# Kernel optimization log

Hardware: AMD Instinct MI355X
Metric: run time of the kernel (lower is better)

Reference implementation:

```python
import jax, jax.numpy as jnp
import numpy as np

B, L = 2048, 120            # batch, sentence length
V, P = 114042, 102          # word vocab, position vocab
WE, PE = 50, 5              # word / position embedding dims
F, K, R = 230, 3, 53        # filters, kernel size, relations
D = WE + 2 * PE             # feature dim = 60


def setup_inputs() -> dict:
    key = jax.random.key(0)
    ks = jax.random.split(key, 10)
    sent = jax.random.randint(ks[0], (B, L), 0, V)
    pf = jax.random.randint(ks[1], (B, 2, L), 0, P)
    # entity positions: ensure 1 <= pool0 < pool1 <= L-1 so all 3 segments are non-empty
    p0 = jax.random.randint(ks[2], (B,), 3, 40)
    p1 = jax.random.randint(ks[3], (B,), 60, 115)
    epos = jnp.stack([p0, p1], axis=1) - 1  # forward uses pool = epos + 1
    s = 0.02
    W_word = jax.random.normal(ks[4], (V, WE), jnp.float32) * s
    W_pos1 = jax.random.normal(ks[5], (P, PE), jnp.float32) * s
    W_pos2 = jax.random.normal(ks[6], (P, PE), jnp.float32) * s
    conv_w = jax.random.normal(ks[7], (F, 1, K, D), jnp.float32) * s
    conv_b = jnp.zeros((F,), jnp.float32)
    lin_w = jax.random.normal(ks[8], (R, 3 * F), jnp.float32) * s
    lin_b = jnp.zeros((R,), jnp.float32)
    return dict(sent=sent, pf=pf, epos=epos, W_word=W_word, W_pos1=W_pos1,
                W_pos2=W_pos2, conv_w=conv_w, conv_b=conv_b, lin_w=lin_w, lin_b=lin_b)


def reference(sent, pf, epos, W_word, W_pos1, W_pos2, conv_w, conv_b, lin_w, lin_b):
    # embeddings -> [B, L, D]
    emb = jnp.concatenate([W_word[sent], W_pos1[pf[:, 0]], W_pos2[pf[:, 1]]], axis=-1)
    # conv over (length, feature) with full-width kernel; dropout is identity (eval)
    x = emb[:, None, :, :]  # [B, 1, L, D]
    y = jax.lax.conv_general_dilated(x, conv_w, window_strides=(1, 1),
                                     padding=[(K // 2, K // 2), (0, 0)])  # [B, F, L, 1]
    y = jnp.tanh(y[..., 0] + conv_b[None, :, None])  # [B, F, L]
    # piecewise (3-segment) max pooling, segment boundaries per batch item
    pool = epos + 1                                   # [B, 2]
    pos = jnp.arange(L)[None, :]                      # [1, L]
    seg = (pos >= pool[:, :1]).astype(jnp.int32) + (pos >= pool[:, 1:]).astype(jnp.int32)  # [B, L] in {0,1,2}
    neg = jnp.finfo(y.dtype).min
    pooled = [jnp.max(jnp.where((seg == s)[:, None, :], y, neg), axis=2) for s in range(3)]
    feats = jnp.stack(pooled, axis=-1).reshape(B, F * 3)  # matches torch cat+view ordering
    return feats @ lin_w.T + lin_b  # [B, R]
```

## Files before the change

kernel.cpp:

```cpp
#include <hip/hip_runtime.h>
#include <math.h>

#define BB 2048
#define LL 120
#define WE_ 50
#define PE_ 5
#define DD 60
#define FF 230
#define KK 3
#define RR 53

#define NKT 6
#define NNT 15
#define NPAD 240
#define EMB_ELEMS 7936

#define WS_BP    0
#define WS_LT    92160
#define WS_EMBG  246784

#define ACC_BIAS 16.0f

#define GATHER_ITEMS (BB * LL * 30)
#define GATHER_BLKS  (GATHER_ITEMS / 256)
#define BP_ITEMS     (NNT * NKT * 64 * 8)
#define LT_ITEMS     (690 * 56)
#define PREP_BLKS    ((BP_ITEMS + LT_ITEMS + 255) / 256)

typedef __attribute__((ext_vector_type(8))) short short8_t;
typedef __attribute__((ext_vector_type(4))) short short4_t;
typedef __attribute__((ext_vector_type(4))) float float4_t;

__device__ __forceinline__ unsigned f2bf(float x) {
    unsigned u = __builtin_bit_cast(unsigned, x);
    return (u + 0x7fffu + ((u >> 16) & 1u)) >> 16;
}

__device__ __forceinline__ float tanh_fast(float x) {
    float t = __expf(2.0f * x);
    return 1.0f - 2.0f * __builtin_amdgcn_rcpf(t + 1.0f);
}

__global__ __launch_bounds__(256) void pcnn_gp(
    const int* __restrict__ sent, const int* __restrict__ pf,
    const float* __restrict__ Wword, const float* __restrict__ Wpos1,
    const float* __restrict__ Wpos2, const float* __restrict__ convw,
    const float* __restrict__ linw,
    unsigned* __restrict__ embg32, unsigned short* __restrict__ bp,
    float* __restrict__ lt)
{
    int bid = blockIdx.x;
    if (bid < GATHER_BLKS) {
        int idx = bid * 256 + threadIdx.x;
        int c  = idx % 30;
        int lc = idx / 30;
        int l  = lc % LL;
        int b  = lc / LL;
        unsigned pk;
        if (c < 25) {
            int w = sent[b * LL + l];
            float2 v = *(const float2*)(Wword + w * WE_ + 2 * c);
            pk = f2bf(v.x) | (f2bf(v.y) << 16);
        } else {
            int p = pf[b * 2 * LL + l];
            int q = pf[b * 2 * LL + LL + l];
            int j0 = (c - 25) * 2, j1 = j0 + 1;
            float f0 = (j0 < PE_) ? Wpos1[p * PE_ + j0] : Wpos2[q * PE_ + j0 - PE_];
            float f1 = (j1 < PE_) ? Wpos1[p * PE_ + j1] : Wpos2[q * PE_ + j1 - PE_];
            pk = f2bf(f0) | (f2bf(f1) << 16);
        }
        embg32[idx] = pk;
    } else {
        int idx = (bid - GATHER_BLKS) * 256 + threadIdx.x;
        if (idx < BP_ITEMS) {
            int j    = idx & 7;
            int lane = (idx >> 3) & 63;
            int t    = idx >> 9;
            int kt   = t % NKT;
            int nt   = t / NKT;
            int f    = nt * 16 + (lane & 15);
            int klin = kt * 32 + (lane >> 4) * 8 + j;
            float v = (f < FF && klin < KK * DD) ? convw[f * (KK * DD) + klin] : 0.0f;
            bp[idx] = (unsigned short)f2bf(v);
        } else if (idx < BP_ITEMS + LT_ITEMS) {
            int k = idx - BP_ITEMS;
            int i = k / 56;
            int r = k - i * 56;
            lt[k] = (r < RR) ? linw[r * (3 * FF) + i] : 0.0f;
        }
    }
}

__global__ __launch_bounds__(256) void pcnn_mfma(
    const int* __restrict__ epos,
    const unsigned short* __restrict__ embg,
    const unsigned short* __restrict__ bp, const float* __restrict__ convb,
    const float* __restrict__ linw_t, const float* __restrict__ linb,
    float* __restrict__ out)
{
    __shared__ __align__(16) union SM {
        unsigned short emb[EMB_ELEMS];
        float pool[4 * NPAD * 3 + NPAD * 3 + 4 * 56];
    } sm;
    unsigned* const keys  = (unsigned*)sm.pool;
    float* const feats    = sm.pool + 4 * NPAD * 3;
    float* const part2    = sm.pool + 4 * NPAD * 3 + NPAD * 3;

    const int b    = blockIdx.x;
    const int tid  = threadIdx.x;
    const int wid  = tid >> 6;
    const int lane = tid & 63;

    const int pool0 = epos[b * 2 + 0] + 1;
    const int pool1 = epos[b * 2 + 1] + 1;

    {
        unsigned* e32 = (unsigned*)sm.emb;
        for (int i = tid; i < 32 + 336; i += 256) {
            int d = (i < 32) ? i : (3600 + i);
            e32[d] = 0u;
        }
    }
    {
        const unsigned short* eb = embg + (size_t)b * (LL * DD);
        #pragma unroll
        for (int k = 0; k < 4; ++k) {
            int c = tid + k * 256;
            if (c < 900) {
                float4 v = *(const float4*)(eb + c * 8);
                *(float4*)((char*)sm.emb + 128 + c * 16) = v;
            }
        }
    }
    __syncthreads();

    short8_t afrag[2][NKT];
    #pragma unroll
    for (int tm2 = 0; tm2 < 2; ++tm2) {
        int l = (2 * wid + tm2) * 16 + (lane & 15);
        #pragma unroll
        for (int kt = 0; kt < NKT; ++kt) {
            int e = l * DD + 4 + kt * 32 + (lane >> 4) * 8;
            short4_t lo = *(const short4_t*)(sm.emb + e);
            short4_t hi = *(const short4_t*)(sm.emb + e + 4);
            short8_t f8;
            f8[0] = lo[0]; f8[1] = lo[1]; f8[2] = lo[2]; f8[3] = lo[3];
            f8[4] = hi[0]; f8[5] = hi[1]; f8[6] = hi[2]; f8[7] = hi[3];
            afrag[tm2][kt] = f8;
        }
    }
    __syncthreads();

    for (int i = tid; i < NPAD * 3; i += 256) keys[i] = 0u;

    const int qrow = (lane >> 4) * 4;
    const int fcol = lane & 15;
    int off[2][4];
    #pragma unroll
    for (int tm2 = 0; tm2 < 2; ++tm2) {
        #pragma unroll
        for (int r = 0; r < 4; ++r) {
            int l = wid * 32 + tm2 * 16 + qrow + r;
            int seg = (l >= pool0) + (l >= pool1);
            off[tm2][r] = fcol * 3 + seg;
        }
    }
    const bool same0 = (off[0][0] == off[0][3]);
    const bool same1 = (off[1][0] == off[1][3]);
    const bool skip_hi = (wid == 3) && (lane >= 32);
    __syncthreads();

    const short8_t* bpv = (const short8_t*)bp;
    short8_t bA[NKT], bB[NKT];
    #pragma unroll
    for (int kt = 0; kt < NKT; ++kt) bA[kt] = bpv[kt * 64 + lane];

    for (int nt = 0; nt < NNT; ++nt) {
        if (nt + 1 < NNT) {
            const short8_t* bn = bpv + (size_t)(nt + 1) * NKT * 64;
            #pragma unroll
            for (int kt = 0; kt < NKT; ++kt) bB[kt] = bn[kt * 64 + lane];
        }

        float4_t acc0 = {0.f, 0.f, 0.f, 0.f};
        float4_t acc1 = {0.f, 0.f, 0.f, 0.f};
        #pragma unroll
        for (int kt = 0; kt < NKT; ++kt) {
            acc0 = __builtin_amdgcn_mfma_f32_16x16x32_bf16(afrag[0][kt], bA[kt], acc0, 0, 0, 0);
            acc1 = __builtin_amdgcn_mfma_f32_16x16x32_bf16(afrag[1][kt], bA[kt], acc1, 0, 0, 0);
        }

        unsigned* kb = keys + nt * 48;
        if (same0) {
            float m = fmaxf(fmaxf(acc0[0], acc0[1]), fmaxf(acc0[2], acc0[3]));
            atomicMax(&kb[off[0][0]], __builtin_bit_cast(unsigned, m + ACC_BIAS));
        } else {
            #pragma unroll
            for (int r = 0; r < 4; ++r)
                atomicMax(&kb[off[0][r]], __builtin_bit_cast(unsigned, acc0[r] + ACC_BIAS));
        }
        if (!skip_hi) {
            if (same1) {
                float m = fmaxf(fmaxf(acc1[0], acc1[1]), fmaxf(acc1[2], acc1[3]));
                atomicMax(&kb[off[1][0]], __builtin_bit_cast(unsigned, m + ACC_BIAS));
            } else {
                #pragma unroll
                for (int r = 0; r < 4; ++r)
                    atomicMax(&kb[off[1][r]], __builtin_bit_cast(unsigned, acc1[r] + ACC_BIAS));
            }
        }

        #pragma unroll
        for (int kt = 0; kt < NKT; ++kt) bA[kt] = bB[kt];
    }
    __syncthreads();

    for (int i = tid; i < FF * 3; i += 256) {
        float m = __builtin_bit_cast(float, keys[i]) - ACC_BIAS;
        int f = i / 3;
        feats[i] = tanh_fast(m + convb[f]);
    }
    __syncthreads();

    {
        int i0 = (690 * wid) >> 2;
        int i1 = (690 * (wid + 1)) >> 2;
        float acc = 0.0f;
        if (lane < 56) {
            #pragma unroll 4
            for (int i = i0; i < i1; ++i)
                acc += feats[i] * linw_t[i * 56 + lane];
            part2[wid * 56 + lane] = acc;
        }
    }
    __syncthreads();
    if (tid < RR) {
        float s = part2[tid] + part2[56 + tid] + part2[112 + tid] + part2[168 + tid];
        out[b * RR + tid] = s + linb[tid];
    }
}

extern "C" void kernel_launch(void* const* d_in, const int* in_sizes, int n_in,
                              void* d_out, int out_size, void* d_ws, size_t ws_size,
                              hipStream_t stream) {
    const int*   sent  = (const int*)d_in[0];
    const int*   pf    = (const int*)d_in[1];
    const int*   epos  = (const int*)d_in[2];
    const float* Wword = (const float*)d_in[3];
    const float* Wpos1 = (const float*)d_in[4];
    const float* Wpos2 = (const float*)d_in[5];
    const float* convw = (const float*)d_in[6];
    const float* convb = (const float*)d_in[7];
    const float* linw  = (const float*)d_in[8];
    const float* linb  = (const float*)d_in[9];
    float* out = (float*)d_out;

    char* ws = (char*)d_ws;
    unsigned short* bp     = (unsigned short*)(ws + WS_BP);
    float*          linw_t = (float*)(ws + WS_LT);
    unsigned short* embg   = (unsigned short*)(ws + WS_EMBG);

    pcnn_gp<<<GATHER_BLKS + PREP_BLKS, 256, 0, stream>>>(
        sent, pf, Wword, Wpos1, Wpos2, convw, linw,
        (unsigned*)embg, bp, linw_t);
    pcnn_mfma<<<BB, 256, 0, stream>>>(epos, embg, bp, convb, linw_t, linb, out);
}
```

Measured before the change: 165.6 us.

## Split conv kernel into 512-thread conv and separate GEMV kernel

The fused per-sentence kernel becomes two kernels. The conv kernel uses 512 threads, with two wave groups each handling half of the filter tiles (8 and 7 tiles), and it drops the double-buffered B-fragment prefetch. Pooled tanh features are written over the sentence's own slot in the embedding workspace, and a second 256-thread kernel reads them back and does the linear layer. This adds parallelism within each block, but costs an extra launch and a global round trip, and every block now stages the same embeddings with only half the MFMA work per wave.

```diff
diff --git a/kernel.cpp b/kernel.cpp
--- a/kernel.cpp
+++ b/kernel.cpp
@@ -91,24 +91,21 @@
     }
 }
 
-__global__ __launch_bounds__(256) void pcnn_mfma(
+__global__ __launch_bounds__(512) void pcnn_conv(
     const int* __restrict__ epos,
-    const unsigned short* __restrict__ embg,
-    const unsigned short* __restrict__ bp, const float* __restrict__ convb,
-    const float* __restrict__ linw_t, const float* __restrict__ linb,
-    float* __restrict__ out)
+    unsigned short* __restrict__ embg,
+    const unsigned short* __restrict__ bp, const float* __restrict__ convb)
 {
     __shared__ __align__(16) union SM {
         unsigned short emb[EMB_ELEMS];
-        float pool[4 * NPAD * 3 + NPAD * 3 + 4 * 56];
+        unsigned keys[NPAD * 3];
     } sm;
-    unsigned* const keys  = (unsigned*)sm.pool;
-    float* const feats    = sm.pool + 4 * NPAD * 3;
-    float* const part2    = sm.pool + 4 * NPAD * 3 + NPAD * 3;
 
     const int b    = blockIdx.x;
     const int tid  = threadIdx.x;
-    const int wid  = tid >> 6;
+    const int wid8 = tid >> 6;
+    const int wid4 = wid8 & 3;
+    const int grp  = wid8 >> 2;
     const int lane = tid & 63;
 
     const int pool0 = epos[b * 2 + 0] + 1;
@@ -116,7 +113,7 @@
 
     {
         unsigned* e32 = (unsigned*)sm.emb;
-        for (int i = tid; i < 32 + 336; i += 256) {
+        for (int i = tid; i < 32 + 336; i += 512) {
             int d = (i < 32) ? i : (3600 + i);
             e32[d] = 0u;
         }
@@ -124,8 +121,8 @@
     {
         const unsigned short* eb = embg + (size_t)b * (LL * DD);
         #pragma unroll
-        for (int k = 0; k < 4; ++k) {
-            int c = tid + k * 256;
+        for (int k = 0; k < 2; ++k) {
+            int c = tid + k * 512;
             if (c < 900) {
                 float4 v = *(const float4*)(eb + c * 8);
                 *(float4*)((char*)sm.emb + 128 + c * 16) = v;
@@ -137,7 +134,7 @@
     short8_t afrag[2][NKT];
     #pragma unroll
     for (int tm2 = 0; tm2 < 2; ++tm2) {
-        int l = (2 * wid + tm2) * 16 + (lane & 15);
+        int l = (2 * wid4 + tm2) * 16 + (lane & 15);
         #pragma unroll
         for (int kt = 0; kt < NKT; ++kt) {
             int e = l * DD + 4 + kt * 32 + (lane >> 4) * 8;
@@ -151,7 +148,7 @@
     }
     __syncthreads();
 
-    for (int i = tid; i < NPAD * 3; i += 256) keys[i] = 0u;
+    for (int i = tid; i < NPAD * 3; i += 512) sm.keys[i] = 0u;
 
     const int qrow = (lane >> 4) * 4;
     const int fcol = lane & 15;
@@ -160,37 +157,34 @@
     for (int tm2 = 0; tm2 < 2; ++tm2) {
         #pragma unroll
         for (int r = 0; r < 4; ++r) {
-            int l = wid * 32 + tm2 * 16 + qrow + r;
+            int l = wid4 * 32 + tm2 * 16 + qrow + r;
             int seg = (l >= pool0) + (l >= pool1);
             off[tm2][r] = fcol * 3 + seg;
         }
     }
     const bool same0 = (off[0][0] == off[0][3]);
     const bool same1 = (off[1][0] == off[1][3]);
-    const bool skip_hi = (wid == 3) && (lane >= 32);
-    __syncthreads();
-
+    const bool skip_hi = (wid4 == 3) && (lane >= 32);
+    __syncthreads();
+
+    const int nt0 = grp ? 8 : 0;
+    const int nt1 = grp ? NNT : 8;
     const short8_t* bpv = (const short8_t*)bp;
-    short8_t bA[NKT], bB[NKT];
-    #pragma unroll
-    for (int kt = 0; kt < NKT; ++kt) bA[kt] = bpv[kt * 64 + lane];
-
-    for (int nt = 0; nt < NNT; ++nt) {
-        if (nt + 1 < NNT) {
-            const short8_t* bn = bpv + (size_t)(nt + 1) * NKT * 64;
-            #pragma unroll
-            for (int kt = 0; kt < NKT; ++kt) bB[kt] = bn[kt * 64 + lane];
-        }
+    for (int nt = nt0; nt < nt1; ++nt) {
+        const short8_t* bn = bpv + (size_t)nt * NKT * 64;
+        short8_t bfrag[NKT];
+        #pragma unroll
+        for (int kt = 0; kt < NKT; ++kt) bfrag[kt] = bn[kt * 64 + lane];
 
         float4_t acc0 = {0.f, 0.f, 0.f, 0.f};
         float4_t acc1 = {0.f, 0.f, 0.f, 0.f};
         #pragma unroll
         for (int kt = 0; kt < NKT; ++kt) {
-            acc0 = __builtin_amdgcn_mfma_f32_16x16x32_bf16(afrag[0][kt], bA[kt], acc0, 0, 0, 0);
-            acc1 = __builtin_amdgcn_mfma_f32_16x16x32_bf16(afrag[1][kt], bA[kt], acc1, 0, 0, 0);
-        }
-
-        unsigned* kb = keys + nt * 48;
+            acc0 = __builtin_amdgcn_mfma_f32_16x16x32_bf16(afrag[0][kt], bfrag[kt], acc0, 0, 0, 0);
+            acc1 = __builtin_amdgcn_mfma_f32_16x16x32_bf16(afrag[1][kt], bfrag[kt], acc1, 0, 0, 0);
+        }
+
+        unsigned* kb = sm.keys + nt * 48;
         if (same0) {
             float m = fmaxf(fmaxf(acc0[0], acc0[1]), fmaxf(acc0[2], acc0[3]));
             atomicMax(&kb[off[0][0]], __builtin_bit_cast(unsigned, m + ACC_BIAS));
@@ -209,17 +203,32 @@
                     atomicMax(&kb[off[1][r]], __builtin_bit_cast(unsigned, acc1[r] + ACC_BIAS));
             }
         }
-
-        #pragma unroll
-        for (int kt = 0; kt < NKT; ++kt) bA[kt] = bB[kt];
-    }
-    __syncthreads();
-
-    for (int i = tid; i < FF * 3; i += 256) {
-        float m = __builtin_bit_cast(float, keys[i]) - ACC_BIAS;
+    }
+    __syncthreads();
+
+    float* fo = (float*)(embg + (size_t)b * (LL * DD));
+    for (int i = tid; i < FF * 3; i += 512) {
+        float m = __builtin_bit_cast(float, sm.keys[i]) - ACC_BIAS;
         int f = i / 3;
-        feats[i] = tanh_fast(m + convb[f]);
-    }
+        fo[i] = tanh_fast(m + convb[f]);
+    }
+}
+
+__global__ __launch_bounds__(256) void pcnn_gemv(
+    const unsigned short* __restrict__ embg,
+    const float* __restrict__ linw_t, const float* __restrict__ linb,
+    float* __restrict__ out)
+{
+    __shared__ float feats[FF * 3];
+    __shared__ float part2[4 * 56];
+
+    const int b    = blockIdx.x;
+    const int tid  = threadIdx.x;
+    const int wid  = tid >> 6;
+    const int lane = tid & 63;
+
+    const float* fi = (const float*)(embg + (size_t)b * (LL * DD));
+    for (int i = tid; i < FF * 3; i += 256) feats[i] = fi[i];
     __syncthreads();
 
     {
@@ -263,5 +272,6 @@
     pcnn_gp<<<GATHER_BLKS + PREP_BLKS, 256, 0, stream>>>(
         sent, pf, Wword, Wpos1, Wpos2, convw, linw,
         (unsigned*)embg, bp, linw_t);
-    pcnn_mfma<<<BB, 256, 0, stream>>>(epos, embg, bp, convb, linw_t, linb, out);
-}
+    pcnn_conv<<<BB, 512, 0, stream>>>(epos, embg, bp, convb);
+    pcnn_gemv<<<BB, 256, 0, stream>>>(embg, linw_t, linb, out);
+}
```

New measurement: 158.8 us. 1.04x faster.
